# Performance work log

Hardware: AMD Instinct MI355X
Metric: run time of the kernel (lower is better)

The kernel has to match this reference:

```python
import jax, jax.numpy as jnp
import numpy as np

B, T, E, H = 4, 2048, 1024, 16
DH = E // H  # head_size = 64


def setup_inputs() -> dict:
    key = jax.random.key(0)
    ks = jax.random.split(key, 6)
    s_in = 1.0 / np.sqrt(E)
    return {
        "x": jax.random.normal(ks[0], (B, T, E), dtype=jnp.float32),
        "Wq": jax.random.normal(ks[1], (H, E, DH), dtype=jnp.float32) * s_in,
        "Wk": jax.random.normal(ks[2], (H, E, DH), dtype=jnp.float32) * s_in,
        "Wv": jax.random.normal(ks[3], (H, E, DH), dtype=jnp.float32) * s_in,
        "Wp": jax.random.normal(ks[4], (E, E), dtype=jnp.float32) * s_in,
        "bp": jax.random.normal(ks[5], (E,), dtype=jnp.float32) * 0.01,
    }


def reference(x, Wq, Wk, Wv, Wp, bp):
    # per-head q/k/v projections, batched over heads: [B,H,T,DH]
    q = jnp.einsum("bte,hed->bhtd", x, Wq)
    k = jnp.einsum("bte,hed->bhtd", x, Wk)
    v = jnp.einsum("bte,hed->bhtd", x, Wv)
    scale = 1.0 / jnp.sqrt(jnp.asarray(DH, dtype=x.dtype))
    scores = jnp.einsum("bhsd,bhtd->bhst", q, k) * scale  # [B,H,T,T]
    causal = jnp.tril(jnp.ones((T, T), dtype=bool))
    scores = jnp.where(causal, scores, jnp.asarray(-jnp.inf, dtype=scores.dtype))
    att = jax.nn.softmax(scores, axis=-1)
    out = jnp.einsum("bhst,bhtd->bhsd", att, v)  # [B,H,T,DH]
    # concat heads along last dim -> [B,T,E]
    out = out.transpose(0, 2, 1, 3).reshape(B, T, E)
    # output projection (dropout p=0.0 is identity)
    return out @ Wp.T + bp
```

## Files before the change

kernel.cpp:

```cpp
#include <hip/hip_runtime.h>
#include <hip/hip_bf16.h>

#define B_ 4
#define T_ 2048
#define E_ 1024
#define H_ 16
#define DH_ 64

typedef __bf16 bf16x8 __attribute__((ext_vector_type(8)));
typedef __bf16 bf16x4 __attribute__((ext_vector_type(4)));
typedef float f32x4 __attribute__((ext_vector_type(4)));

#define EXP2F(x) __builtin_amdgcn_exp2f(x)
#define NEG_INF (-__builtin_inff())

__device__ __forceinline__ void async_copy16(const __bf16* g, __bf16* l) {
    __builtin_amdgcn_global_load_lds(
        (const __attribute__((address_space(1))) unsigned int*)g,
        (__attribute__((address_space(3))) unsigned int*)l, 16, 0, 0);
}

__global__ void cast_all(const float* __restrict__ x,
                         const float* __restrict__ Wq, const float* __restrict__ Wk,
                         const float* __restrict__ Wv, const float* __restrict__ Wp,
                         __bf16* __restrict__ xb, __bf16* __restrict__ wcat,
                         __bf16* __restrict__ wpb) {
    int tid = blockIdx.x * blockDim.x + threadIdx.x;
    {
        int i = tid * 4;
        float4 f = *reinterpret_cast<const float4*>(x + i);
        bf16x4 o = { (__bf16)f.x, (__bf16)f.y, (__bf16)f.z, (__bf16)f.w };
        *reinterpret_cast<bf16x4*>(xb + i) = o;
    }
    if (tid < 262144) {
        int i = tid * 4;
        float4 f = *reinterpret_cast<const float4*>(Wp + i);
        bf16x4 o = { (__bf16)f.x, (__bf16)f.y, (__bf16)f.z, (__bf16)f.w };
        *reinterpret_cast<bf16x4*>(wpb + i) = o;
    }
    if (tid < 786432) {
        int i = tid * 4;
        int e = i & (E_ - 1);
        int n = i >> 10;
        int rem = n & 1023, h = rem >> 6, d = rem & 63;
        const float* src = (n < 1024) ? Wq : (n < 2048 ? Wk : Wv);
        const float* sp = src + ((long)((h << 10) + e)) * DH_ + d;
        bf16x4 o = { (__bf16)sp[0], (__bf16)sp[DH_], (__bf16)sp[2 * DH_], (__bf16)sp[3 * DH_] };
        *reinterpret_cast<bf16x4*>(wcat + i) = o;
    }
}

template<int MODE>
__global__ __launch_bounds__(256, 3) void gemm128(
    const __bf16* __restrict__ A, const __bf16* __restrict__ Bt,
    float* __restrict__ Cf, const float* __restrict__ bias,
    __bf16* __restrict__ oq, __bf16* __restrict__ ok, __bf16* __restrict__ ovt,
    int K, int N) {

    __shared__ __bf16 As[128][64];
    __shared__ __bf16 Bs[128][64];

    int tid = threadIdx.x, lane = tid & 63, wid = tid >> 6;
    int wr = wid >> 1, wc = wid & 1;
    int rlo = lane & 15, rhi = lane >> 4;
    int l8 = lane >> 3, c = lane & 7;

    const __bf16* Ab = A + (long)blockIdx.x * 128 * K;
    const __bf16* Bb = Bt + (long)blockIdx.y * 128 * K;

    f32x4 acc[4][4] = {};

    for (int k0 = 0; k0 < K; k0 += 64) {
        #pragma unroll
        for (int p = 0; p < 4; p++) {
            int gr = p * 32 + wid * 8 + l8;
            int sc = c ^ (gr & 7);
            async_copy16(Ab + (long)gr * K + k0 + sc * 8, &As[p * 32 + wid * 8][0]);
        }
        #pragma unroll
        for (int p = 0; p < 4; p++) {
            int gr = p * 32 + wid * 8 + l8;
            int sc = c ^ (gr & 7);
            async_copy16(Bb + (long)gr * K + k0 + sc * 8, &Bs[p * 32 + wid * 8][0]);
        }
        __syncthreads();

        #pragma unroll
        for (int kk = 0; kk < 2; kk++) {
            bf16x8 af[4], bfr[4];
            #pragma unroll
            for (int mi = 0; mi < 4; mi++) {
                int r = wr * 64 + mi * 16 + rlo;
                af[mi] = *reinterpret_cast<const bf16x8*>(
                    &As[r][((kk * 4 + rhi) ^ (r & 7)) * 8]);
            }
            #pragma unroll
            for (int ni = 0; ni < 4; ni++) {
                int r = wc * 64 + ni * 16 + rlo;
                bfr[ni] = *reinterpret_cast<const bf16x8*>(
                    &Bs[r][((kk * 4 + rhi) ^ (r & 7)) * 8]);
            }
            #pragma unroll
            for (int mi = 0; mi < 4; mi++)
                #pragma unroll
                for (int ni = 0; ni < 4; ni++)
                    acc[mi][ni] = __builtin_amdgcn_mfma_f32_16x16x32_bf16(
                        af[mi], bfr[ni], acc[mi][ni], 0, 0, 0);
        }
        __syncthreads();
    }

    long m0 = (long)blockIdx.x * 128 + wr * 64;
    int n0 = blockIdx.y * 128 + wc * 64;

    if constexpr (MODE == 1) {
        #pragma unroll
        for (int mi = 0; mi < 4; mi++) {
            #pragma unroll
            for (int ni = 0; ni < 4; ni++) {
                int cn = n0 + ni * 16 + rlo;
                #pragma unroll
                for (int r = 0; r < 4; r++) {
                    long rm = m0 + mi * 16 + rhi * 4 + r;
                    Cf[rm * N + cn] = acc[mi][ni][r] + bias[cn];
                }
            }
        }
    } else {
        int type = blockIdx.y >> 3;
        #pragma unroll
        for (int mi = 0; mi < 4; mi++) {
            long m_ = m0 + mi * 16 + rhi * 4;
            int b = (int)(m_ >> 11);
            int t0 = (int)(m_ & 2047);
            #pragma unroll
            for (int ni = 0; ni < 4; ni++) {
                int n = n0 + ni * 16 + rlo;
                int rem = n & 1023, h = rem >> 6, d = rem & 63;
                long bh = b * 16 + h;
                if (type == 2) {
                    bf16x4 o = { (__bf16)acc[mi][ni][0], (__bf16)acc[mi][ni][1],
                                 (__bf16)acc[mi][ni][2], (__bf16)acc[mi][ni][3] };
                    *reinterpret_cast<bf16x4*>(ovt + (bh * 64 + d) * 2048 + t0) = o;
                } else {
                    __bf16* dst = (type ? ok : oq) + bh * 2048 * 64;
                    #pragma unroll
                    for (int r = 0; r < 4; r++)
                        dst[(long)(t0 + r) * 64 + d] = (__bf16)acc[mi][ni][r];
                }
            }
        }
    }
}

__global__ __launch_bounds__(256, 4) void attn_kernel(
    const __bf16* __restrict__ q, const __bf16* __restrict__ k,
    const __bf16* __restrict__ vt, __bf16* __restrict__ attout) {

    __shared__ __bf16 Ks[2][64][64];
    __shared__ __bf16 Vs[2][64][64];
    __shared__ __bf16 Pl[4][16][64];

    int tid = threadIdx.x, lane = tid & 63, wid = tid >> 6;
    int rlo = lane & 15, rhi = lane >> 4;

    int fid = blockIdx.y * 16 + blockIdx.x;
    int xcd = fid & 7, slot = fid >> 3;
    int bh = xcd * 8 + (slot >> 4);
    int p = slot & 15;
    int tA = 31 - p, tB = p;

    int b = bh >> 4, h = bh & 15;
    const __bf16* qb = q + (long)bh * T_ * DH_;
    const __bf16* kb = k + (long)bh * T_ * DH_;
    const __bf16* vtb = vt + (long)bh * T_ * DH_;

    const float SCL = 0.125f * 1.44269504088896340736f;

    int srow = wid * 16 + (lane >> 3);
    int sc0 = (lane & 7) ^ (srow & 7);

    bf16x8 aqA[2], aqB[2];
    {
        long qrA = (long)tA * 64 + wid * 16 + rlo;
        aqA[0] = *reinterpret_cast<const bf16x8*>(qb + qrA * DH_ + 8 * rhi);
        aqA[1] = *reinterpret_cast<const bf16x8*>(qb + qrA * DH_ + 32 + 8 * rhi);
        long qrB = (long)tB * 64 + wid * 16 + rlo;
        aqB[0] = *reinterpret_cast<const bf16x8*>(qb + qrB * DH_ + 8 * rhi);
        aqB[1] = *reinterpret_cast<const bf16x8*>(qb + qrB * DH_ + 32 + 8 * rhi);
    }

    float mA = NEG_INF, lAc = 0.f, mB = NEG_INF, lBc = 0.f;
    f32x4 oA[4] = {}, oB[4] = {};

    auto STAGE = [&](int bs, int t) {
        const __bf16* ksrc = kb + (long)(t * 64 + srow) * DH_ + sc0 * 8;
        async_copy16(ksrc,           &Ks[bs][wid * 16][0]);
        async_copy16(ksrc + 8 * DH_, &Ks[bs][wid * 16 + 8][0]);
        const __bf16* vsrc = vtb + (long)srow * T_ + t * 64 + sc0 * 8;
        async_copy16(vsrc,           &Vs[bs][wid * 16][0]);
        async_copy16(vsrc + 8 * T_,  &Vs[bs][wid * 16 + 8][0]);
    };

    auto APPLYMASK = [&](f32x4* s, int qrow, int kt0) {
        int kbase = kt0 + rhi * 4;
        #pragma unroll
        for (int f = 0; f < 4; f++)
            #pragma unroll
            for (int r = 0; r < 4; r++)
                if (kbase + f * 16 + r > qrow) s[f][r] = NEG_INF;
    };

    auto SOFTMAX_PV = [&](int bs, f32x4* s, float& m_, float& l_, f32x4* o) {
        f32x4 mx;
        #pragma unroll
        for (int r = 0; r < 4; r++)
            mx[r] = fmaxf(fmaxf(s[0][r], s[1][r]), fmaxf(s[2][r], s[3][r]));
        float pml = fmaxf(fmaxf(mx[0], mx[1]), fmaxf(mx[2], mx[3]));
        float pms = pml * SCL;

        bool need = !__all(pms <= m_ + 8.f);
        if (need) {
            float pr = fmaxf(pms, __shfl_xor(pms, 16));
            pr = fmaxf(pr, __shfl_xor(pr, 32));
            float nm = fmaxf(m_, pr);
            float so = EXP2F(m_ - nm);
            m_ = nm;
            l_ *= so;
            float sov[4];
            #pragma unroll
            for (int r = 0; r < 4; r++) sov[r] = __shfl(so, rhi * 4 + r);
            #pragma unroll
            for (int fd = 0; fd < 4; fd++)
                #pragma unroll
                for (int r = 0; r < 4; r++)
                    o[fd][r] *= sov[r];
        }

        float rsum = 0.f;
        #pragma unroll
        for (int f = 0; f < 4; f++)
            #pragma unroll
            for (int r = 0; r < 4; r++) {
                float pv = EXP2F(fmaf(s[f][r], SCL, -m_));
                s[f][r] = pv;
                rsum += pv;
            }
        l_ += rsum;

        #pragma unroll
        for (int f = 0; f < 4; f++) {
            bf16x4 pw = { (__bf16)s[f][0], (__bf16)s[f][1],
                          (__bf16)s[f][2], (__bf16)s[f][3] };
            int keyb = f * 16 + rhi * 4;
            int c16 = keyb >> 3, sub = (keyb >> 2) & 1;
            *reinterpret_cast<bf16x4*>(
                &Pl[wid][rlo][((c16 ^ (rlo & 7)) << 3) + (sub << 2)]) = pw;
        }

        __builtin_amdgcn_s_setprio(1);
        #pragma unroll
        for (int kk = 0; kk < 2; kk++) {
            int ck = kk * 4 + rhi;
            bf16x8 ap = *reinterpret_cast<const bf16x8*>(&Pl[wid][rlo][(ck ^ (rlo & 7)) * 8]);
            #pragma unroll
            for (int fd = 0; fd < 4; fd++) {
                int vr = fd * 16 + rlo;
                bf16x8 bv = *reinterpret_cast<const bf16x8*>(
                    &Vs[bs][vr][(ck ^ (vr & 7)) * 8]);
                o[fd] = __builtin_amdgcn_mfma_f32_16x16x32_bf16(ap, bv, o[fd], 0, 0, 0);
            }
        }
        __builtin_amdgcn_s_setprio(0);
    };

    int qrowA = tA * 64 + wid * 16 + rlo;
    int qrowB = tB * 64 + wid * 16 + rlo;

    int nsteps = tA + 1;

    STAGE(0, 0);
    STAGE(1, 1);
    asm volatile("s_waitcnt vmcnt(4)" ::: "memory");
    asm volatile("s_barrier" ::: "memory");

    for (int t = 0; t < nsteps; ++t) {
        int cur = t & 1;
        bool doB = (t <= tB);

        f32x4 sA[4], sB[4];
        __builtin_amdgcn_s_setprio(1);
        #pragma unroll
        for (int f = 0; f < 4; f++) {
            int kr = f * 16 + rlo;
            bf16x8 ak0 = *reinterpret_cast<const bf16x8*>(
                &Ks[cur][kr][((0 + rhi) ^ (kr & 7)) * 8]);
            bf16x8 ak1 = *reinterpret_cast<const bf16x8*>(
                &Ks[cur][kr][((4 + rhi) ^ (kr & 7)) * 8]);
            f32x4 a0 = {};
            a0 = __builtin_amdgcn_mfma_f32_16x16x32_bf16(ak0, aqA[0], a0, 0, 0, 0);
            a0 = __builtin_amdgcn_mfma_f32_16x16x32_bf16(ak1, aqA[1], a0, 0, 0, 0);
            sA[f] = a0;
            if (doB) {
                f32x4 b0 = {};
                b0 = __builtin_amdgcn_mfma_f32_16x16x32_bf16(ak0, aqB[0], b0, 0, 0, 0);
                b0 = __builtin_amdgcn_mfma_f32_16x16x32_bf16(ak1, aqB[1], b0, 0, 0, 0);
                sB[f] = b0;
            }
        }
        __builtin_amdgcn_s_setprio(0);

        if (t == tA) APPLYMASK(sA, qrowA, t * 64);
        SOFTMAX_PV(cur, sA, mA, lAc, oA);
        if (doB) {
            if (t == tB) APPLYMASK(sB, qrowB, t * 64);
            SOFTMAX_PV(cur, sB, mB, lBc, oB);
        }

        asm volatile("s_barrier" ::: "memory");
        if (t + 2 < nsteps) {
            STAGE(cur, t + 2);
            asm volatile("s_waitcnt vmcnt(4)" ::: "memory");
        } else {
            asm volatile("s_waitcnt vmcnt(0)" ::: "memory");
        }
        asm volatile("s_barrier" ::: "memory");
    }

    lAc += __shfl_xor(lAc, 16);
    lAc += __shfl_xor(lAc, 32);
    lBc += __shfl_xor(lBc, 16);
    lBc += __shfl_xor(lBc, 32);

    float lvA[4], lvB[4];
    #pragma unroll
    for (int r = 0; r < 4; r++) {
        lvA[r] = __shfl(lAc, rhi * 4 + r);
        lvB[r] = __shfl(lBc, rhi * 4 + r);
    }
    #pragma unroll
    for (int r = 0; r < 4; r++) {
        float invA = 1.f / lvA[r];
        float invB = 1.f / lvB[r];
        long qrA = (long)tA * 64 + wid * 16 + rhi * 4 + r;
        long qrB = (long)tB * 64 + wid * 16 + rhi * 4 + r;
        #pragma unroll
        for (int fd = 0; fd < 4; fd++) {
            int d = fd * 16 + rlo;
            attout[((long)b * T_ + qrA) * E_ + h * DH_ + d] = (__bf16)(oA[fd][r] * invA);
            attout[((long)b * T_ + qrB) * E_ + h * DH_ + d] = (__bf16)(oB[fd][r] * invB);
        }
    }
}

extern "C" void kernel_launch(void* const* d_in, const int* in_sizes, int n_in,
                              void* d_out, int out_size, void* d_ws, size_t ws_size,
                              hipStream_t stream) {
    const float* x  = (const float*)d_in[0];
    const float* Wq = (const float*)d_in[1];
    const float* Wk = (const float*)d_in[2];
    const float* Wv = (const float*)d_in[3];
    const float* Wp = (const float*)d_in[4];
    const float* bp = (const float*)d_in[5];

    char* ws = (char*)d_ws;
    const long SZ_XE = (long)B_ * T_ * E_ * 2;
    __bf16* xb   = (__bf16*)(ws);
    __bf16* qb   = (__bf16*)(ws + SZ_XE);
    __bf16* kb   = (__bf16*)(ws + 2 * SZ_XE);
    __bf16* vt   = (__bf16*)(ws + 3 * SZ_XE);
    __bf16* wcat = (__bf16*)(ws + 4 * SZ_XE);
    __bf16* wpb  = (__bf16*)(ws + 4 * SZ_XE + (long)3072 * 1024 * 2);
    __bf16* att  = xb;

    cast_all<<<8192, 256, 0, stream>>>(x, Wq, Wk, Wv, Wp, xb, wcat, wpb);

    gemm128<3><<<dim3(64, 24), 256, 0, stream>>>(
        xb, wcat, nullptr, nullptr, qb, kb, vt, E_, 3 * E_);

    attn_kernel<<<dim3(16, B_ * H_), 256, 0, stream>>>(qb, kb, vt, att);

    gemm128<1><<<dim3(64, 8), 256, 0, stream>>>(
        att, wpb, (float*)d_out, bp, nullptr, nullptr, nullptr, E_, E_);
}
```

Measured before the change: 158.8 us.

## Feed softmax probabilities directly from registers into PV MFMA via 16x16x16 instruction

Drops the per-wave LDS staging buffer for the probability tile. The probabilities produced in the S accumulator layout now feed the P·V product directly as operands of the 16x16x16 bf16 MFMA, and V is read from LDS in matching 4-element chunks. Each V fragment load is shared between the A and B query tiles. This removes an LDS write/read round trip per step, but uses twice as many, smaller MFMA instructions in place of the 16x16x32 ones, plus narrower 8-byte LDS reads of V.

```diff
diff --git a/kernel.cpp b/kernel.cpp
--- a/kernel.cpp
+++ b/kernel.cpp
@@ -9,6 +9,7 @@
 
 typedef __bf16 bf16x8 __attribute__((ext_vector_type(8)));
 typedef __bf16 bf16x4 __attribute__((ext_vector_type(4)));
+typedef short short4b __attribute__((ext_vector_type(4)));
 typedef float f32x4 __attribute__((ext_vector_type(4)));
 
 #define EXP2F(x) __builtin_amdgcn_exp2f(x)
@@ -159,7 +160,6 @@
 
     __shared__ __bf16 Ks[2][64][64];
     __shared__ __bf16 Vs[2][64][64];
-    __shared__ __bf16 Pl[4][16][64];
 
     int tid = threadIdx.x, lane = tid & 63, wid = tid >> 6;
     int rlo = lane & 15, rhi = lane >> 4;
@@ -211,7 +211,7 @@
                 if (kbase + f * 16 + r > qrow) s[f][r] = NEG_INF;
     };
 
-    auto SOFTMAX_PV = [&](int bs, f32x4* s, float& m_, float& l_, f32x4* o) {
+    auto SM_CVT = [&](f32x4* s, float& m_, float& l_, f32x4* o, short4b* pA) {
         f32x4 mx;
         #pragma unroll
         for (int r = 0; r < 4; r++)
@@ -239,39 +239,17 @@
 
         float rsum = 0.f;
         #pragma unroll
-        for (int f = 0; f < 4; f++)
+        for (int f = 0; f < 4; f++) {
+            f32x4 pv;
             #pragma unroll
             for (int r = 0; r < 4; r++) {
-                float pv = EXP2F(fmaf(s[f][r], SCL, -m_));
-                s[f][r] = pv;
-                rsum += pv;
-            }
+                pv[r] = EXP2F(fmaf(s[f][r], SCL, -m_));
+                rsum += pv[r];
+            }
+            bf16x4 pw = { (__bf16)pv[0], (__bf16)pv[1], (__bf16)pv[2], (__bf16)pv[3] };
+            pA[f] = __builtin_bit_cast(short4b, pw);
+        }
         l_ += rsum;
-
-        #pragma unroll
-        for (int f = 0; f < 4; f++) {
-            bf16x4 pw = { (__bf16)s[f][0], (__bf16)s[f][1],
-                          (__bf16)s[f][2], (__bf16)s[f][3] };
-            int keyb = f * 16 + rhi * 4;
-            int c16 = keyb >> 3, sub = (keyb >> 2) & 1;
-            *reinterpret_cast<bf16x4*>(
-                &Pl[wid][rlo][((c16 ^ (rlo & 7)) << 3) + (sub << 2)]) = pw;
-        }
-
-        __builtin_amdgcn_s_setprio(1);
-        #pragma unroll
-        for (int kk = 0; kk < 2; kk++) {
-            int ck = kk * 4 + rhi;
-            bf16x8 ap = *reinterpret_cast<const bf16x8*>(&Pl[wid][rlo][(ck ^ (rlo & 7)) * 8]);
-            #pragma unroll
-            for (int fd = 0; fd < 4; fd++) {
-                int vr = fd * 16 + rlo;
-                bf16x8 bv = *reinterpret_cast<const bf16x8*>(
-                    &Vs[bs][vr][(ck ^ (vr & 7)) * 8]);
-                o[fd] = __builtin_amdgcn_mfma_f32_16x16x32_bf16(ap, bv, o[fd], 0, 0, 0);
-            }
-        }
-        __builtin_amdgcn_s_setprio(0);
     };
 
     int qrowA = tA * 64 + wid * 16 + rlo;
@@ -311,11 +289,27 @@
         __builtin_amdgcn_s_setprio(0);
 
         if (t == tA) APPLYMASK(sA, qrowA, t * 64);
-        SOFTMAX_PV(cur, sA, mA, lAc, oA);
-        if (doB) {
-            if (t == tB) APPLYMASK(sB, qrowB, t * 64);
-            SOFTMAX_PV(cur, sB, mB, lBc, oB);
-        }
+        if (doB && t == tB) APPLYMASK(sB, qrowB, t * 64);
+
+        short4b pAa[4], pAb[4];
+        SM_CVT(sA, mA, lAc, oA, pAa);
+        if (doB) SM_CVT(sB, mB, lBc, oB, pAb);
+
+        __builtin_amdgcn_s_setprio(1);
+        #pragma unroll
+        for (int f = 0; f < 4; f++) {
+            #pragma unroll
+            for (int fd = 0; fd < 4; fd++) {
+                int d = fd * 16 + rlo;
+                int c = 2 * f + (rhi >> 1);
+                const __bf16* vp = &Vs[cur][d][((c ^ (d & 7)) << 3) + (rhi & 1) * 4];
+                short4b vB = *reinterpret_cast<const short4b*>(vp);
+                oA[fd] = __builtin_amdgcn_mfma_f32_16x16x16bf16_1k(pAa[f], vB, oA[fd], 0, 0, 0);
+                if (doB)
+                    oB[fd] = __builtin_amdgcn_mfma_f32_16x16x16bf16_1k(pAb[f], vB, oB[fd], 0, 0, 0);
+            }
+        }
+        __builtin_amdgcn_s_setprio(0);
 
         asm volatile("s_barrier" ::: "memory");
         if (t + 2 < nsteps) {
```

After: 164.9 us. 3.9% more time.

## Share K/V tiles between two query-pair groups in 512-thread attention blocks

Applied to the files above, without the earlier changes.

Attention blocks grow to 512 threads as two 4-wave groups, each owning one balanced causal query-tile pair (p and 31-p) from adjacent pairs. Both groups share a single staged K/V tile, so each K/V tile is fetched from global memory once for two pairs, and each thread issues half the async copies. The cost is that the group with the shorter range sits idle at barriers on its final step. Bigger blocks may also reduce occupancy and make scheduling coarser.

```diff
diff --git a/kernel.cpp b/kernel.cpp
--- a/kernel.cpp
+++ b/kernel.cpp
@@ -153,21 +153,24 @@
     }
 }
 
-__global__ __launch_bounds__(256, 4) void attn_kernel(
+__global__ __launch_bounds__(512, 4) void attn_kernel(
     const __bf16* __restrict__ q, const __bf16* __restrict__ k,
     const __bf16* __restrict__ vt, __bf16* __restrict__ attout) {
 
     __shared__ __bf16 Ks[2][64][64];
     __shared__ __bf16 Vs[2][64][64];
-    __shared__ __bf16 Pl[4][16][64];
+    __shared__ __bf16 Pl[8][16][64];
 
     int tid = threadIdx.x, lane = tid & 63, wid = tid >> 6;
+    int wg = wid >> 2;
+    int wl = wid & 3;
     int rlo = lane & 15, rhi = lane >> 4;
 
-    int fid = blockIdx.y * 16 + blockIdx.x;
+    int fid = blockIdx.y * 8 + blockIdx.x;
     int xcd = fid & 7, slot = fid >> 3;
-    int bh = xcd * 8 + (slot >> 4);
-    int p = slot & 15;
+    int bh = xcd * 8 + (slot >> 3);
+    int pi = slot & 7;
+    int p = 2 * pi + wg;
     int tA = 31 - p, tB = p;
 
     int b = bh >> 4, h = bh & 15;
@@ -177,15 +180,15 @@
 
     const float SCL = 0.125f * 1.44269504088896340736f;
 
-    int srow = wid * 16 + (lane >> 3);
+    int srow = wid * 8 + (lane >> 3);
     int sc0 = (lane & 7) ^ (srow & 7);
 
     bf16x8 aqA[2], aqB[2];
     {
-        long qrA = (long)tA * 64 + wid * 16 + rlo;
+        long qrA = (long)tA * 64 + wl * 16 + rlo;
         aqA[0] = *reinterpret_cast<const bf16x8*>(qb + qrA * DH_ + 8 * rhi);
         aqA[1] = *reinterpret_cast<const bf16x8*>(qb + qrA * DH_ + 32 + 8 * rhi);
-        long qrB = (long)tB * 64 + wid * 16 + rlo;
+        long qrB = (long)tB * 64 + wl * 16 + rlo;
         aqB[0] = *reinterpret_cast<const bf16x8*>(qb + qrB * DH_ + 8 * rhi);
         aqB[1] = *reinterpret_cast<const bf16x8*>(qb + qrB * DH_ + 32 + 8 * rhi);
     }
@@ -194,12 +197,8 @@
     f32x4 oA[4] = {}, oB[4] = {};
 
     auto STAGE = [&](int bs, int t) {
-        const __bf16* ksrc = kb + (long)(t * 64 + srow) * DH_ + sc0 * 8;
-        async_copy16(ksrc,           &Ks[bs][wid * 16][0]);
-        async_copy16(ksrc + 8 * DH_, &Ks[bs][wid * 16 + 8][0]);
-        const __bf16* vsrc = vtb + (long)srow * T_ + t * 64 + sc0 * 8;
-        async_copy16(vsrc,           &Vs[bs][wid * 16][0]);
-        async_copy16(vsrc + 8 * T_,  &Vs[bs][wid * 16 + 8][0]);
+        async_copy16(kb + (long)(t * 64 + srow) * DH_ + sc0 * 8, &Ks[bs][wid * 8][0]);
+        async_copy16(vtb + (long)srow * T_ + t * 64 + sc0 * 8,   &Vs[bs][wid * 8][0]);
     };
 
     auto APPLYMASK = [&](f32x4* s, int qrow, int kt0) {
@@ -211,7 +210,7 @@
                 if (kbase + f * 16 + r > qrow) s[f][r] = NEG_INF;
     };
 
-    auto SOFTMAX_PV = [&](int bs, f32x4* s, float& m_, float& l_, f32x4* o) {
+    auto SM_PACK = [&](f32x4* s, float& m_, float& l_, f32x4* o) {
         f32x4 mx;
         #pragma unroll
         for (int r = 0; r < 4; r++)
@@ -257,7 +256,9 @@
             *reinterpret_cast<bf16x4*>(
                 &Pl[wid][rlo][((c16 ^ (rlo & 7)) << 3) + (sub << 2)]) = pw;
         }
-
+    };
+
+    auto PV = [&](int bs, f32x4* o) {
         __builtin_amdgcn_s_setprio(1);
         #pragma unroll
         for (int kk = 0; kk < 2; kk++) {
@@ -274,53 +275,59 @@
         __builtin_amdgcn_s_setprio(0);
     };
 
-    int qrowA = tA * 64 + wid * 16 + rlo;
-    int qrowB = tB * 64 + wid * 16 + rlo;
-
-    int nsteps = tA + 1;
+    int qrowA = tA * 64 + wl * 16 + rlo;
+    int qrowB = tB * 64 + wl * 16 + rlo;
+
+    int nsteps = 32 - 2 * pi;
 
     STAGE(0, 0);
     STAGE(1, 1);
-    asm volatile("s_waitcnt vmcnt(4)" ::: "memory");
+    asm volatile("s_waitcnt vmcnt(2)" ::: "memory");
     asm volatile("s_barrier" ::: "memory");
 
     for (int t = 0; t < nsteps; ++t) {
         int cur = t & 1;
+        bool doA = (t <= tA);
         bool doB = (t <= tB);
 
-        f32x4 sA[4], sB[4];
-        __builtin_amdgcn_s_setprio(1);
-        #pragma unroll
-        for (int f = 0; f < 4; f++) {
-            int kr = f * 16 + rlo;
-            bf16x8 ak0 = *reinterpret_cast<const bf16x8*>(
-                &Ks[cur][kr][((0 + rhi) ^ (kr & 7)) * 8]);
-            bf16x8 ak1 = *reinterpret_cast<const bf16x8*>(
-                &Ks[cur][kr][((4 + rhi) ^ (kr & 7)) * 8]);
-            f32x4 a0 = {};
-            a0 = __builtin_amdgcn_mfma_f32_16x16x32_bf16(ak0, aqA[0], a0, 0, 0, 0);
-            a0 = __builtin_amdgcn_mfma_f32_16x16x32_bf16(ak1, aqA[1], a0, 0, 0, 0);
-            sA[f] = a0;
+        if (doA) {
+            f32x4 sA[4], sB[4];
+            __builtin_amdgcn_s_setprio(1);
+            #pragma unroll
+            for (int f = 0; f < 4; f++) {
+                int kr = f * 16 + rlo;
+                bf16x8 ak0 = *reinterpret_cast<const bf16x8*>(
+                    &Ks[cur][kr][((0 + rhi) ^ (kr & 7)) * 8]);
+                bf16x8 ak1 = *reinterpret_cast<const bf16x8*>(
+                    &Ks[cur][kr][((4 + rhi) ^ (kr & 7)) * 8]);
+                f32x4 a0 = {};
+                a0 = __builtin_amdgcn_mfma_f32_16x16x32_bf16(ak0, aqA[0], a0, 0, 0, 0);
+                a0 = __builtin_amdgcn_mfma_f32_16x16x32_bf16(ak1, aqA[1], a0, 0, 0, 0);
+                sA[f] = a0;
+                if (doB) {
+                    f32x4 b0 = {};
+                    b0 = __builtin_amdgcn_mfma_f32_16x16x32_bf16(ak0, aqB[0], b0, 0, 0, 0);
+                    b0 = __builtin_amdgcn_mfma_f32_16x16x32_bf16(ak1, aqB[1], b0, 0, 0, 0);
+                    sB[f] = b0;
+                }
+            }
+            __builtin_amdgcn_s_setprio(0);
+
+            if (t == tA) APPLYMASK(sA, qrowA, t * 64);
+            if (doB && t == tB) APPLYMASK(sB, qrowB, t * 64);
+
+            SM_PACK(sA, mA, lAc, oA);
+            PV(cur, oA);
             if (doB) {
-                f32x4 b0 = {};
-                b0 = __builtin_amdgcn_mfma_f32_16x16x32_bf16(ak0, aqB[0], b0, 0, 0, 0);
-                b0 = __builtin_amdgcn_mfma_f32_16x16x32_bf16(ak1, aqB[1], b0, 0, 0, 0);
-                sB[f] = b0;
-            }
-        }
-        __builtin_amdgcn_s_setprio(0);
-
-        if (t == tA) APPLYMASK(sA, qrowA, t * 64);
-        SOFTMAX_PV(cur, sA, mA, lAc, oA);
-        if (doB) {
-            if (t == tB) APPLYMASK(sB, qrowB, t * 64);
-            SOFTMAX_PV(cur, sB, mB, lBc, oB);
+                SM_PACK(sB, mB, lBc, oB);
+                PV(cur, oB);
+            }
         }
 
         asm volatile("s_barrier" ::: "memory");
         if (t + 2 < nsteps) {
             STAGE(cur, t + 2);
-            asm volatile("s_waitcnt vmcnt(4)" ::: "memory");
+            asm volatile("s_waitcnt vmcnt(2)" ::: "memory");
         } else {
             asm volatile("s_waitcnt vmcnt(0)" ::: "memory");
         }
@@ -342,8 +349,8 @@
     for (int r = 0; r < 4; r++) {
         float invA = 1.f / lvA[r];
         float invB = 1.f / lvB[r];
-        long qrA = (long)tA * 64 + wid * 16 + rhi * 4 + r;
-        long qrB = (long)tB * 64 + wid * 16 + rhi * 4 + r;
+        long qrA = (long)tA * 64 + wl * 16 + rhi * 4 + r;
+        long qrB = (long)tB * 64 + wl * 16 + rhi * 4 + r;
         #pragma unroll
         for (int fd = 0; fd < 4; fd++) {
             int d = fd * 16 + rlo;
@@ -378,7 +385,7 @@
     gemm128<3><<<dim3(64, 24), 256, 0, stream>>>(
         xb, wcat, nullptr, nullptr, qb, kb, vt, E_, 3 * E_);
 
-    attn_kernel<<<dim3(16, B_ * H_), 256, 0, stream>>>(qb, kb, vt, att);
+    attn_kernel<<<dim3(8, B_ * H_), 512, 0, stream>>>(qb, kb, vt, att);
 
     gemm128<1><<<dim3(64, 8), 256, 0, stream>>>(
         att, wpb, (float*)d_out, bp, nullptr, nullptr, nullptr, E_, E_);
```

Result: slower. 162.8 us (+2.5%).

## Use 256x128 GEMM tiles with triple-buffered async LDS pipeline

Applied to the files above, without the earlier changes.

Replaces the 128x128 single-buffered GEMM with a 256x128 tile run by 8 waves, backed by a three-stage LDS ring. Global-to-LDS async loads for tile t+2 are interleaved with the MFMA phases of tile t, and a single barrier per iteration is gated on vmcnt waits. MFMA sections are raised in priority with s_setprio. The aim is to hide global load latency and halve the barriers per k-step. In exchange, LDS use grows to about 144KB per block, so fewer blocks can be resident, and the grid shrinks to half as many blocks.

```diff
diff --git a/kernel.cpp b/kernel.cpp
--- a/kernel.cpp
+++ b/kernel.cpp
@@ -51,67 +51,92 @@
 }
 
 template<int MODE>
-__global__ __launch_bounds__(256, 3) void gemm128(
+__global__ __launch_bounds__(512, 2) void gemm256(
     const __bf16* __restrict__ A, const __bf16* __restrict__ Bt,
     float* __restrict__ Cf, const float* __restrict__ bias,
     __bf16* __restrict__ oq, __bf16* __restrict__ ok, __bf16* __restrict__ ovt,
     int K, int N) {
 
-    __shared__ __bf16 As[128][64];
-    __shared__ __bf16 Bs[128][64];
+    __shared__ __bf16 As[3][256][64];
+    __shared__ __bf16 Bs[3][128][64];
 
     int tid = threadIdx.x, lane = tid & 63, wid = tid >> 6;
-    int wr = wid >> 1, wc = wid & 1;
+    int wm = wid >> 1, wn = wid & 1;
     int rlo = lane & 15, rhi = lane >> 4;
-    int l8 = lane >> 3, c = lane & 7;
-
-    const __bf16* Ab = A + (long)blockIdx.x * 128 * K;
+    int srow8 = tid >> 3;
+    int sc = tid & 7;
+
+    const __bf16* Ab = A + (long)blockIdx.x * 256 * K;
     const __bf16* Bb = Bt + (long)blockIdx.y * 128 * K;
 
     f32x4 acc[4][4] = {};
-
-    for (int k0 = 0; k0 < K; k0 += 64) {
-        #pragma unroll
-        for (int p = 0; p < 4; p++) {
-            int gr = p * 32 + wid * 8 + l8;
-            int sc = c ^ (gr & 7);
-            async_copy16(Ab + (long)gr * K + k0 + sc * 8, &As[p * 32 + wid * 8][0]);
-        }
-        #pragma unroll
-        for (int p = 0; p < 4; p++) {
-            int gr = p * 32 + wid * 8 + l8;
-            int sc = c ^ (gr & 7);
-            async_copy16(Bb + (long)gr * K + k0 + sc * 8, &Bs[p * 32 + wid * 8][0]);
-        }
-        __syncthreads();
-
-        #pragma unroll
-        for (int kk = 0; kk < 2; kk++) {
-            bf16x8 af[4], bfr[4];
-            #pragma unroll
-            for (int mi = 0; mi < 4; mi++) {
-                int r = wr * 64 + mi * 16 + rlo;
-                af[mi] = *reinterpret_cast<const bf16x8*>(
-                    &As[r][((kk * 4 + rhi) ^ (r & 7)) * 8]);
-            }
-            #pragma unroll
-            for (int ni = 0; ni < 4; ni++) {
-                int r = wc * 64 + ni * 16 + rlo;
-                bfr[ni] = *reinterpret_cast<const bf16x8*>(
-                    &Bs[r][((kk * 4 + rhi) ^ (r & 7)) * 8]);
-            }
-            #pragma unroll
-            for (int mi = 0; mi < 4; mi++)
-                #pragma unroll
-                for (int ni = 0; ni < 4; ni++)
-                    acc[mi][ni] = __builtin_amdgcn_mfma_f32_16x16x32_bf16(
-                        af[mi], bfr[ni], acc[mi][ni], 0, 0, 0);
-        }
-        __syncthreads();
-    }
-
-    long m0 = (long)blockIdx.x * 128 + wr * 64;
-    int n0 = blockIdx.y * 128 + wc * 64;
+    int NT = K >> 6;
+
+    auto STAGE_A = [&](int buf, int t, int g) {
+        int gr = g * 64 + srow8;
+        int scs = sc ^ (gr & 7);
+        async_copy16(Ab + (long)gr * K + t * 64 + scs * 8, &As[buf][g * 64 + wid * 8][0]);
+    };
+    auto STAGE_B = [&](int buf, int t, int g) {
+        int gr = g * 64 + srow8;
+        int scs = sc ^ (gr & 7);
+        async_copy16(Bb + (long)gr * K + t * 64 + scs * 8, &Bs[buf][g * 64 + wid * 8][0]);
+    };
+
+    auto PHASE = [&](int buf, int kk) {
+        bf16x8 af[4], bf[4];
+        #pragma unroll
+        for (int mi = 0; mi < 4; mi++) {
+            int r = wm * 64 + mi * 16 + rlo;
+            af[mi] = *reinterpret_cast<const bf16x8*>(
+                &As[buf][r][((kk * 4 + rhi) ^ (r & 7)) * 8]);
+        }
+        #pragma unroll
+        for (int ni = 0; ni < 4; ni++) {
+            int rn = wn * 64 + ni * 16 + rlo;
+            bf[ni] = *reinterpret_cast<const bf16x8*>(
+                &Bs[buf][rn][((kk * 4 + rhi) ^ (rn & 7)) * 8]);
+        }
+        __builtin_amdgcn_s_setprio(1);
+        #pragma unroll
+        for (int mi = 0; mi < 4; mi++)
+            #pragma unroll
+            for (int ni = 0; ni < 4; ni++)
+                acc[mi][ni] = __builtin_amdgcn_mfma_f32_16x16x32_bf16(
+                    af[mi], bf[ni], acc[mi][ni], 0, 0, 0);
+        __builtin_amdgcn_s_setprio(0);
+    };
+
+    #pragma unroll
+    for (int g = 0; g < 4; g++) STAGE_A(0, 0, g);
+    #pragma unroll
+    for (int g = 0; g < 2; g++) STAGE_B(0, 0, g);
+    #pragma unroll
+    for (int g = 0; g < 4; g++) STAGE_A(1, 1, g);
+    #pragma unroll
+    for (int g = 0; g < 2; g++) STAGE_B(1, 1, g);
+    asm volatile("s_waitcnt vmcnt(6)" ::: "memory");
+    asm volatile("s_barrier" ::: "memory");
+
+    for (int t = 0; t < NT; ++t) {
+        int buf = t % 3;
+        int nbuf = (t + 2) % 3;
+        bool pre = (t + 2 < NT);
+
+        if (pre) { STAGE_A(nbuf, t + 2, 0); STAGE_A(nbuf, t + 2, 1); STAGE_B(nbuf, t + 2, 0); }
+        PHASE(buf, 0);
+        if (pre) { STAGE_A(nbuf, t + 2, 2); STAGE_A(nbuf, t + 2, 3); STAGE_B(nbuf, t + 2, 1); }
+        PHASE(buf, 1);
+
+        if (t + 1 < NT) {
+            if (pre) asm volatile("s_waitcnt vmcnt(6)" ::: "memory");
+            else     asm volatile("s_waitcnt vmcnt(0)" ::: "memory");
+            asm volatile("s_barrier" ::: "memory");
+        }
+    }
+
+    long m0 = (long)blockIdx.x * 256 + wm * 64;
+    int n0 = blockIdx.y * 128 + wn * 64;
 
     if constexpr (MODE == 1) {
         #pragma unroll
@@ -127,7 +152,7 @@
             }
         }
     } else {
-        int type = blockIdx.y >> 3;
+        int type = n0 >> 10;
         #pragma unroll
         for (int mi = 0; mi < 4; mi++) {
             long m_ = m0 + mi * 16 + rhi * 4;
@@ -375,11 +400,11 @@
 
     cast_all<<<8192, 256, 0, stream>>>(x, Wq, Wk, Wv, Wp, xb, wcat, wpb);
 
-    gemm128<3><<<dim3(64, 24), 256, 0, stream>>>(
+    gemm256<3><<<dim3(32, 24), 512, 0, stream>>>(
         xb, wcat, nullptr, nullptr, qb, kb, vt, E_, 3 * E_);
 
     attn_kernel<<<dim3(16, B_ * H_), 256, 0, stream>>>(qb, kb, vt, att);
 
-    gemm128<1><<<dim3(64, 8), 256, 0, stream>>>(
+    gemm256<1><<<dim3(32, 8), 512, 0, stream>>>(
         att, wpb, (float*)d_out, bp, nullptr, nullptr, nullptr, E_, E_);
 }
```

New measurement: 190.4 us. 1.2x slower.
